# Performance work log

Hardware: AMD Instinct MI355X
Metric: run time of the kernel (lower is better)

The kernel has to match this reference:

```python
import jax, jax.numpy as jnp
import numpy as np

N_NODES = 50000
N_EDGES = 1250000
VOCAB = 50000
EMBED = 64
HIDDEN = 64
NUM_REL = 3
N_CLASSES = 2
N_GRAPHS = 512


def setup_inputs() -> dict:
    key = jax.random.key(0)
    ks = jax.random.split(key, 12)
    x = jax.random.randint(ks[0], (N_NODES,), 0, VOCAB, dtype=jnp.int32)
    edge_index = jax.random.randint(ks[1], (2, N_EDGES), 0, N_NODES, dtype=jnp.int32)
    edge_type = jax.random.randint(ks[2], (N_EDGES,), 0, NUM_REL, dtype=jnp.int32)
    batch = jnp.sort(jax.random.randint(ks[3], (N_NODES,), 0, N_GRAPHS, dtype=jnp.int32))
    s = 0.05
    emb = jax.random.normal(ks[4], (VOCAB, EMBED), jnp.float32) * s
    w1_rel = jax.random.normal(ks[5], (NUM_REL, EMBED, HIDDEN), jnp.float32) * s
    w1_root = jax.random.normal(ks[6], (EMBED, HIDDEN), jnp.float32) * s
    b1 = jnp.zeros((HIDDEN,), jnp.float32)
    w2_rel = jax.random.normal(ks[7], (NUM_REL, HIDDEN, HIDDEN), jnp.float32) * s
    w2_root = jax.random.normal(ks[8], (HIDDEN, HIDDEN), jnp.float32) * s
    b2 = jnp.zeros((HIDDEN,), jnp.float32)
    lin_w = jax.random.normal(ks[9], (HIDDEN, N_CLASSES), jnp.float32) * s
    lin_b = jnp.zeros((N_CLASSES,), jnp.float32)
    return {"x": x, "edge_index": edge_index, "edge_type": edge_type, "batch": batch,
            "emb": emb, "w1_rel": w1_rel, "w1_root": w1_root, "b1": b1,
            "w2_rel": w2_rel, "w2_root": w2_root, "b2": b2,
            "lin_w": lin_w, "lin_b": lin_b}


def rgcn_conv(h, src, dst, edge_type, w_rel, w_root, bias):
    # PyG RGCNConv: out = h @ W_root + bias + sum_r mean-aggregated (h_src @ W_r)
    out = h @ w_root + bias
    h_src = h[src]  # [E, F] gather
    for r in range(NUM_REL):
        mask = (edge_type == r).astype(h.dtype)  # [E]
        m = (h_src @ w_rel[r]) * mask[:, None]   # [E, H]
        s = jax.ops.segment_sum(m, dst, num_segments=N_NODES)
        cnt = jax.ops.segment_sum(mask, dst, num_segments=N_NODES)
        out = out + s / jnp.maximum(cnt, 1.0)[:, None]
    return out


def reference(x, edge_index, edge_type, batch, emb, w1_rel, w1_root, b1,
              w2_rel, w2_root, b2, lin_w, lin_b):
    src, dst = edge_index[0], edge_index[1]
    emb_eff = emb.at[0].set(0.0)  # padding_idx=0
    h = emb_eff[x]  # [N, EMBED]
    h = jax.nn.relu(rgcn_conv(h, src, dst, edge_type, w1_rel, w1_root, b1))
    h = jax.nn.relu(rgcn_conv(h, src, dst, edge_type, w2_rel, w2_root, b2))
    # global mean pool over graphs
    sums = jax.ops.segment_sum(h, batch, num_segments=N_GRAPHS)
    cnt = jax.ops.segment_sum(jnp.ones((h.shape[0],), h.dtype), batch, num_segments=N_GRAPHS)
    pooled = sums / jnp.maximum(cnt, 1.0)[:, None]  # [G, HIDDEN]
    return pooled @ lin_w + lin_b  # [G, N_CLASSES]
```

## Files before the change

kernel.cpp:

```cpp
#include <hip/hip_runtime.h>

#define CHUNK 2048

__global__ __launch_bounds__(256) void embed_count_kernel(
    const int* __restrict__ x, const float* __restrict__ emb, float* __restrict__ h0,
    const int* __restrict__ ei, int* __restrict__ pcount,
    int n_nodes, int n_edges, int n_bkt, int embed_blocks)
{
    __shared__ int cnt[512];
    int t = threadIdx.x;
    if ((int)blockIdx.x < embed_blocks) {
        int tt = blockIdx.x * 256 + t;
        if (tt < n_nodes * 16) {
            int n = tt >> 4, q = tt & 15;
            int xv = x[n];
            float4 v = {0.f, 0.f, 0.f, 0.f};
            if (xv != 0) v = *(const float4*)(emb + (size_t)xv * 64 + q * 4);
            *(float4*)(h0 + (size_t)n * 64 + q * 4) = v;
        }
        return;
    }
    int jb = blockIdx.x - embed_blocks;
    for (int b = t; b < 512; b += 256) cnt[b] = 0;
    __syncthreads();
    int base = jb * CHUNK;
#pragma unroll
    for (int i = 0; i < CHUNK / 256; ++i) {
        int e = base + i * 256 + t;
        if (e < n_edges) atomicAdd(&cnt[ei[n_edges + e] >> 7], 1);
    }
    __syncthreads();
    for (int b = t; b < n_bkt; b += 256) pcount[jb * n_bkt + b] = cnt[b];
}

__global__ __launch_bounds__(256) void colscan_kernel(
    const int* __restrict__ pcount, int* __restrict__ pre,
    int* __restrict__ totals, int* __restrict__ rowstartR,
    const int* __restrict__ batch, const float* __restrict__ linb,
    float* __restrict__ inv_cnt, float* __restrict__ outg,
    int n_chk, int n_bkt, int n_edges, int n_nodes, int n_graphs)
{
    __shared__ int ps[256];
    int b = blockIdx.x, t = threadIdx.x;
    if (b >= n_bkt) {
        int g = (b - n_bkt) * 256 + t;
        if (g < n_graphs) {
            int lo = 0, hi = n_nodes;
            while (lo < hi) { int mid = (lo + hi) >> 1; if (batch[mid] < g) lo = mid + 1; else hi = mid; }
            int s = lo;
            lo = 0; hi = n_nodes;
            while (lo < hi) { int mid = (lo + hi) >> 1; if (batch[mid] < g + 1) lo = mid + 1; else hi = mid; }
            inv_cnt[g] = 1.f / (float)max(lo - s, 1);
            outg[2 * g + 0] = linb[0];
            outg[2 * g + 1] = linb[1];
        }
        return;
    }
    if (b == 0 && t == 0) rowstartR[4 * n_nodes] = n_edges;
    int v[4], s = 0;
#pragma unroll
    for (int i = 0; i < 4; ++i) {
        int jj = t * 4 + i;
        v[i] = (jj < n_chk) ? pcount[jj * n_bkt + b] : 0;
        s += v[i];
    }
    ps[t] = s;
    __syncthreads();
    for (int o = 1; o < 256; o <<= 1) {
        int u = (t >= o) ? ps[t - o] : 0;
        __syncthreads();
        ps[t] += u;
        __syncthreads();
    }
    int run = (t > 0) ? ps[t - 1] : 0;
#pragma unroll
    for (int i = 0; i < 4; ++i) {
        int jj = t * 4 + i;
        if (jj < n_chk) pre[jj * n_bkt + b] = run;
        run += v[i];
    }
    if (t == 255) totals[b] = run;
}

__global__ __launch_bounds__(256) void scatter_kernel(
    const int* __restrict__ ei, const int* __restrict__ et,
    const int* __restrict__ pre, const int* __restrict__ totals,
    int* __restrict__ esort, int* __restrict__ bucket_start,
    int n_edges, int n_bkt)
{
    __shared__ int bs[512], fill2[512], ps[256];
    int t = threadIdx.x, j = blockIdx.x;
    int a0 = (2 * t < n_bkt) ? totals[2 * t] : 0;
    int a1 = (2 * t + 1 < n_bkt) ? totals[2 * t + 1] : 0;
    ps[t] = a0 + a1;
    __syncthreads();
    for (int o = 1; o < 256; o <<= 1) {
        int u = (t >= o) ? ps[t - o] : 0;
        __syncthreads();
        ps[t] += u;
        __syncthreads();
    }
    int basex = (t > 0) ? ps[t - 1] : 0;
    bs[2 * t] = basex;
    bs[2 * t + 1] = basex + a0;
    fill2[t] = 0; fill2[t + 256] = 0;
    __syncthreads();
    if (j == 0) {
        for (int b = t; b < n_bkt; b += 256) bucket_start[b] = bs[b];
        if (t == 0) bucket_start[n_bkt] = n_edges;
    }
    for (int b = t; b < n_bkt; b += 256) bs[b] += pre[j * n_bkt + b];
    __syncthreads();
    int base = j * CHUNK;
#pragma unroll
    for (int i = 0; i < CHUNK / 256; ++i) {
        int e = base + i * 256 + t;
        if (e < n_edges) {
            int s = ei[e], d = ei[n_edges + e], r = et[e];
            int b = d >> 7;
            int pos = bs[b] + atomicAdd(&fill2[b], 1);
            esort[pos] = s | (r << 16) | ((d & 127) << 18);
        }
    }
}

__global__ __launch_bounds__(256) void bucket_sort_kernel(
    const int* __restrict__ bucket_start, int* __restrict__ esort,
    int* __restrict__ scratch, int* __restrict__ rowstartR, int n_nodes)
{
    __shared__ int cnt[512], off[512], fill[512], ps[256];
    int t = threadIdx.x, b = blockIdx.x;
    int s = bucket_start[b], e = bucket_start[b + 1];
    cnt[t] = 0; cnt[t + 256] = 0; fill[t] = 0; fill[t + 256] = 0;
    __syncthreads();
    int* scr = scratch + (size_t)b * 8192;
    for (int i = s + t; i < e; i += 256) {
        int p = esort[i];
        scr[i - s] = p;
        atomicAdd(&cnt[(p >> 16) & 0x1FF], 1);
    }
    __syncthreads();
    int a0 = cnt[2 * t], a1 = cnt[2 * t + 1];
    ps[t] = a0 + a1;
    __syncthreads();
    for (int o = 1; o < 256; o <<= 1) {
        int v = (t >= o) ? ps[t - o] : 0;
        __syncthreads();
        ps[t] += v;
        __syncthreads();
    }
    int basex = (t > 0) ? ps[t - 1] : 0;
    off[2 * t] = basex;
    off[2 * t + 1] = basex + a0;
    __syncthreads();
    int d0 = b * 128 + (2 * t >> 2);
    if (d0 < n_nodes) rowstartR[b * 512 + 2 * t] = s + off[2 * t];
    int d1 = b * 128 + ((2 * t + 1) >> 2);
    if (d1 < n_nodes) rowstartR[b * 512 + 2 * t + 1] = s + off[2 * t + 1];
    __syncthreads();
    for (int i = s + t; i < e; i += 256) {
        int p = scr[i - s];
        int bin = (p >> 16) & 0x1FF;
        int pos = s + off[bin] + atomicAdd(&fill[bin], 1);
        esort[pos] = p;
    }
}

__global__ __launch_bounds__(256) void agg_kernel(
    const float* __restrict__ hin, const int* __restrict__ rowstartR,
    const int* __restrict__ esort, float* __restrict__ means, int n_nodes)
{
    int wid = (blockIdx.x * 256 + threadIdx.x) >> 6;
    int lane = threadIdx.x & 63;
    if (wid >= n_nodes) return;
    int q = lane >> 4;
    int c = lane & 15;
    int4 rs = *(const int4*)(rowstartR + wid * 4);
    int s = rs.x, e = rs.w;

    float4 a0 = {0.f,0.f,0.f,0.f}, a1 = {0.f,0.f,0.f,0.f}, a2 = {0.f,0.f,0.f,0.f};

    int i = s + 4 * q;
    for (; i + 4 <= e; i += 16) {
        int p0 = esort[i], p1 = esort[i + 1], p2 = esort[i + 2], p3 = esort[i + 3];
        float4 v0 = *(const float4*)(hin + (size_t)(p0 & 0xFFFF) * 64 + c * 4);
        float4 v1 = *(const float4*)(hin + (size_t)(p1 & 0xFFFF) * 64 + c * 4);
        float4 v2 = *(const float4*)(hin + (size_t)(p2 & 0xFFFF) * 64 + c * 4);
        float4 v3 = *(const float4*)(hin + (size_t)(p3 & 0xFFFF) * 64 + c * 4);
#pragma unroll
        for (int m = 0; m < 4; ++m) {
            int p = m == 0 ? p0 : m == 1 ? p1 : m == 2 ? p2 : p3;
            float4 v = m == 0 ? v0 : m == 1 ? v1 : m == 2 ? v2 : v3;
            int r = (p >> 16) & 3;
            float m0 = (r == 0) ? 1.f : 0.f;
            float m1 = (r == 1) ? 1.f : 0.f;
            float m2 = (r == 2) ? 1.f : 0.f;
            a0.x = fmaf(m0, v.x, a0.x); a0.y = fmaf(m0, v.y, a0.y);
            a0.z = fmaf(m0, v.z, a0.z); a0.w = fmaf(m0, v.w, a0.w);
            a1.x = fmaf(m1, v.x, a1.x); a1.y = fmaf(m1, v.y, a1.y);
            a1.z = fmaf(m1, v.z, a1.z); a1.w = fmaf(m1, v.w, a1.w);
            a2.x = fmaf(m2, v.x, a2.x); a2.y = fmaf(m2, v.y, a2.y);
            a2.z = fmaf(m2, v.z, a2.z); a2.w = fmaf(m2, v.w, a2.w);
        }
    }
#pragma unroll
    for (int m = 0; m < 3; ++m) {
        int ii = i + m;
        if (ii < e) {
            int p = esort[ii];
            float4 v = *(const float4*)(hin + (size_t)(p & 0xFFFF) * 64 + c * 4);
            int r = (p >> 16) & 3;
            float m0 = (r == 0) ? 1.f : 0.f;
            float m1 = (r == 1) ? 1.f : 0.f;
            float m2 = (r == 2) ? 1.f : 0.f;
            a0.x = fmaf(m0, v.x, a0.x); a0.y = fmaf(m0, v.y, a0.y);
            a0.z = fmaf(m0, v.z, a0.z); a0.w = fmaf(m0, v.w, a0.w);
            a1.x = fmaf(m1, v.x, a1.x); a1.y = fmaf(m1, v.y, a1.y);
            a1.z = fmaf(m1, v.z, a1.z); a1.w = fmaf(m1, v.w, a1.w);
            a2.x = fmaf(m2, v.x, a2.x); a2.y = fmaf(m2, v.y, a2.y);
            a2.z = fmaf(m2, v.z, a2.z); a2.w = fmaf(m2, v.w, a2.w);
        }
    }
#pragma unroll
    for (int off = 16; off < 64; off <<= 1) {
        a0.x += __shfl_xor(a0.x, off); a0.y += __shfl_xor(a0.y, off);
        a0.z += __shfl_xor(a0.z, off); a0.w += __shfl_xor(a0.w, off);
        a1.x += __shfl_xor(a1.x, off); a1.y += __shfl_xor(a1.y, off);
        a1.z += __shfl_xor(a1.z, off); a1.w += __shfl_xor(a1.w, off);
        a2.x += __shfl_xor(a2.x, off); a2.y += __shfl_xor(a2.y, off);
        a2.z += __shfl_xor(a2.z, off); a2.w += __shfl_xor(a2.w, off);
    }
    if (q < 3) {
        int cnt = (q == 0) ? (rs.y - rs.x) : (q == 1) ? (rs.z - rs.y) : (rs.w - rs.z);
        float4 a = (q == 0) ? a0 : (q == 1) ? a1 : a2;
        float inv = 1.f / (float)max(cnt, 1);
        float4 m = {a.x * inv, a.y * inv, a.z * inv, a.w * inv};
        *(float4*)(means + (size_t)wid * 192 + q * 64 + c * 4) = m;
    }
}

__global__ __launch_bounds__(256) void transform_kernel(
    const float* __restrict__ hin, const float* __restrict__ means,
    const float* __restrict__ wroot, const float* __restrict__ wrel,
    const float* __restrict__ bias, float* __restrict__ hout,
    const int* __restrict__ batch, const float* __restrict__ linw,
    const float* __restrict__ inv_cnt, float* __restrict__ outg,
    int n_nodes, int do_pool)
{
    __shared__ float wsh[2][4096];
    __shared__ float gacc[64][2];
    int t = threadIdx.x;
    int gt = blockIdx.x * 256 + t;
    int g = gt >> 4, q = gt & 15;
    int n0 = g * 4;
    bool active = (n0 < n_nodes);

    {
        const float4* sp = (const float4*)wroot;
        float4* d = (float4*)wsh[0];
#pragma unroll
        for (int i = 0; i < 4; ++i) d[t + i * 256] = sp[t + i * 256];
    }

    float4 acc[4];
    float4 b = {0.f, 0.f, 0.f, 0.f};
    if (active) b = *(const float4*)(bias + q * 4);
#pragma unroll
    for (int i = 0; i < 4; ++i) acc[i] = b;

    const float* hv = hin + (size_t)n0 * 64;
    const float* mv = means + (size_t)n0 * 192;

    for (int s = 0; s < 4; ++s) {
        __syncthreads();
        if (s < 3) {
            const float4* sp = (const float4*)wrel + (size_t)s * 1024;
            float4* d = (float4*)wsh[(s + 1) & 1];
#pragma unroll
            for (int i = 0; i < 4; ++i) d[t + i * 256] = sp[t + i * 256];
        }
        const float* vbase = (s == 0) ? hv : (mv + (s - 1) * 64);
        int vstride = (s == 0) ? 64 : 192;
        const float* wbuf = wsh[s & 1];
        if (active) {
#pragma unroll 4
            for (int k4 = 0; k4 < 16; ++k4) {
                float4 v[4];
#pragma unroll
                for (int i = 0; i < 4; ++i)
                    v[i] = *(const float4*)(vbase + i * vstride + k4 * 4);
#pragma unroll
                for (int kk = 0; kk < 4; ++kk) {
                    float4 w = *(const float4*)(wbuf + (k4 * 4 + kk) * 64 + q * 4);
#pragma unroll
                    for (int i = 0; i < 4; ++i) {
                        float sv = kk == 0 ? v[i].x : kk == 1 ? v[i].y : kk == 2 ? v[i].z : v[i].w;
                        acc[i].x = fmaf(sv, w.x, acc[i].x);
                        acc[i].y = fmaf(sv, w.y, acc[i].y);
                        acc[i].z = fmaf(sv, w.z, acc[i].z);
                        acc[i].w = fmaf(sv, w.w, acc[i].w);
                    }
                }
            }
        }
    }
    if (!do_pool) {
        if (active) {
            float* o = hout + (size_t)n0 * 64 + q * 4;
#pragma unroll
            for (int i = 0; i < 4; ++i) {
                float4 r = {fmaxf(acc[i].x, 0.f), fmaxf(acc[i].y, 0.f),
                            fmaxf(acc[i].z, 0.f), fmaxf(acc[i].w, 0.f)};
                *(float4*)(o + i * 64) = r;
            }
        }
    } else {
        if (t < 64) { gacc[t][0] = 0.f; gacc[t][1] = 0.f; }
        __syncthreads();
        int nbase = blockIdx.x * 64;
        int gmin = batch[min(nbase, n_nodes - 1)];
        if (active) {
            float4 lwA = *(const float4*)(linw + q * 8);
            float4 lwB = *(const float4*)(linw + q * 8 + 4);
            float d0[4], d1[4];
#pragma unroll
            for (int i = 0; i < 4; ++i) {
                float4 r = {fmaxf(acc[i].x, 0.f), fmaxf(acc[i].y, 0.f),
                            fmaxf(acc[i].z, 0.f), fmaxf(acc[i].w, 0.f)};
                d0[i] = r.x * lwA.x + r.y * lwA.z + r.z * lwB.x + r.w * lwB.z;
                d1[i] = r.x * lwA.y + r.y * lwA.w + r.z * lwB.y + r.w * lwB.w;
            }
#pragma unroll
            for (int off = 1; off < 16; off <<= 1) {
#pragma unroll
                for (int i = 0; i < 4; ++i) {
                    d0[i] += __shfl_xor(d0[i], off);
                    d1[i] += __shfl_xor(d1[i], off);
                }
            }
            if (q == 0) {
#pragma unroll
                for (int i = 0; i < 4; ++i) {
                    int n = n0 + i;
                    if (n < n_nodes) {
                        int gg = batch[n];
                        float ic = inv_cnt[gg];
                        int idx = gg - gmin;
                        if (idx < 64) {
                            atomicAdd(&gacc[idx][0], d0[i] * ic);
                            atomicAdd(&gacc[idx][1], d1[i] * ic);
                        } else {
                            atomicAdd(&outg[2 * gg + 0], d0[i] * ic);
                            atomicAdd(&outg[2 * gg + 1], d1[i] * ic);
                        }
                    }
                }
            }
        }
        __syncthreads();
        if (t < 64) {
            float v0 = gacc[t][0], v1 = gacc[t][1];
            if (v0 != 0.f || v1 != 0.f) {
                atomicAdd(&outg[2 * (gmin + t) + 0], v0);
                atomicAdd(&outg[2 * (gmin + t) + 1], v1);
            }
        }
    }
}

extern "C" void kernel_launch(void* const* d_in, const int* in_sizes, int n_in,
                              void* d_out, int out_size, void* d_ws, size_t ws_size,
                              hipStream_t stream)
{
    const int*   x      = (const int*)d_in[0];
    const int*   ei     = (const int*)d_in[1];
    const int*   et     = (const int*)d_in[2];
    const int*   batch  = (const int*)d_in[3];
    const float* emb    = (const float*)d_in[4];
    const float* w1rel  = (const float*)d_in[5];
    const float* w1root = (const float*)d_in[6];
    const float* b1     = (const float*)d_in[7];
    const float* w2rel  = (const float*)d_in[8];
    const float* w2root = (const float*)d_in[9];
    const float* b2     = (const float*)d_in[10];
    const float* linw   = (const float*)d_in[11];
    const float* linb   = (const float*)d_in[12];
    float* out = (float*)d_out;

    const int N = in_sizes[0];
    const int E = in_sizes[2];
    const int G = out_size / 2;
    const int NBKT = (N + 127) >> 7;
    const int NCHK = (E + CHUNK - 1) / CHUNK;

    float* hA        = (float*)d_ws;
    float* hB        = hA + (size_t)N * 64;
    float* means     = hB + (size_t)N * 64;
    int*   esort     = (int*)(means + (size_t)N * 192);
    int*   rowstartR = esort + E;
    int*   bucket_start = rowstartR + 4 * N + 4;
    int*   totals    = bucket_start + NBKT + 1;
    float* inv_cnt   = (float*)(totals + NBKT);
    int*   scratch   = (int*)means;
    int*   pcount    = (int*)means + 4 * 1024 * 1024;
    int*   pre       = (int*)means + 5 * 1024 * 1024;

    int embedBlocks = (N * 16 + 255) / 256;
    embed_count_kernel<<<embedBlocks + NCHK, 256, 0, stream>>>(
        x, emb, hA, ei, pcount, N, E, NBKT, embedBlocks);
    int gBlocks = (G + 255) / 256;
    colscan_kernel<<<NBKT + gBlocks, 256, 0, stream>>>(
        pcount, pre, totals, rowstartR, batch, linb, inv_cnt, out,
        NCHK, NBKT, E, N, G);
    scatter_kernel<<<NCHK, 256, 0, stream>>>(ei, et, pre, totals, esort, bucket_start, E, NBKT);
    bucket_sort_kernel<<<NBKT, 256, 0, stream>>>(bucket_start, esort, scratch, rowstartR, N);

    int aggBlocks = (N * 64 + 255) / 256;
    int tfBlocks  = ((N + 3) / 4 * 16 + 255) / 256;
    agg_kernel<<<aggBlocks, 256, 0, stream>>>(hA, rowstartR, esort, means, N);
    transform_kernel<<<tfBlocks, 256, 0, stream>>>(
        hA, means, w1root, w1rel, b1, hB, batch, linw, inv_cnt, out, N, 0);
    agg_kernel<<<aggBlocks, 256, 0, stream>>>(hB, rowstartR, esort, means, N);
    transform_kernel<<<tfBlocks, 256, 0, stream>>>(
        hB, means, w2root, w2rel, b2, hA, batch, linw, inv_cnt, out, N, 1);
}
```

Measured before the change: 308.5 us.

## Halve per-thread node tile in transform kernel and stage weights via direct LDS loads

The transform kernel now processes two nodes per 16-thread group instead of four, doubling the block count. Weights are staged in 32-row half-matrices through global_load_lds, which cuts shared memory per block from 32 KB to 16 KB, and the pipeline runs over 8 sub-stages. A launch-bounds occupancy hint of 6 is added. The goal is more occupancy and latency hiding, at the cost of less register reuse of weight loads and twice as many barriers.

```diff
diff --git a/kernel.cpp b/kernel.cpp
--- a/kernel.cpp
+++ b/kernel.cpp
@@ -239,7 +239,15 @@
     }
 }
 
-__global__ __launch_bounds__(256) void transform_kernel(
+__device__ __forceinline__ void stage16(const float* gsrc, float* ldst)
+{
+    __builtin_amdgcn_global_load_lds(
+        (const __attribute__((address_space(1))) unsigned int*)gsrc,
+        (__attribute__((address_space(3))) unsigned int*)ldst,
+        16, 0, 0);
+}
+
+__global__ __launch_bounds__(256, 6) void transform_kernel(
     const float* __restrict__ hin, const float* __restrict__ means,
     const float* __restrict__ wroot, const float* __restrict__ wrel,
     const float* __restrict__ bias, float* __restrict__ hout,
@@ -247,59 +255,58 @@
     const float* __restrict__ inv_cnt, float* __restrict__ outg,
     int n_nodes, int do_pool)
 {
-    __shared__ float wsh[2][4096];
+    __shared__ float wsh[2][2048];
     __shared__ float gacc[64][2];
     int t = threadIdx.x;
     int gt = blockIdx.x * 256 + t;
     int g = gt >> 4, q = gt & 15;
-    int n0 = g * 4;
+    int n0 = g * 2;
     bool active = (n0 < n_nodes);
 
+    stage16(wroot + t * 4,        wsh[0] + t * 4);
+    stage16(wroot + 1024 + t * 4, wsh[0] + 1024 + t * 4);
+
+    float4 acc0, acc1;
     {
-        const float4* sp = (const float4*)wroot;
-        float4* d = (float4*)wsh[0];
-#pragma unroll
-        for (int i = 0; i < 4; ++i) d[t + i * 256] = sp[t + i * 256];
-    }
-
-    float4 acc[4];
-    float4 b = {0.f, 0.f, 0.f, 0.f};
-    if (active) b = *(const float4*)(bias + q * 4);
-#pragma unroll
-    for (int i = 0; i < 4; ++i) acc[i] = b;
+        float4 b = {0.f, 0.f, 0.f, 0.f};
+        if (active) b = *(const float4*)(bias + q * 4);
+        acc0 = b; acc1 = b;
+    }
 
     const float* hv = hin + (size_t)n0 * 64;
     const float* mv = means + (size_t)n0 * 192;
 
-    for (int s = 0; s < 4; ++s) {
-        __syncthreads();
-        if (s < 3) {
-            const float4* sp = (const float4*)wrel + (size_t)s * 1024;
-            float4* d = (float4*)wsh[(s + 1) & 1];
-#pragma unroll
-            for (int i = 0; i < 4; ++i) d[t + i * 256] = sp[t + i * 256];
-        }
-        const float* vbase = (s == 0) ? hv : (mv + (s - 1) * 64);
-        int vstride = (s == 0) ? 64 : 192;
-        const float* wbuf = wsh[s & 1];
+    for (int ss = 0; ss < 8; ++ss) {
+        __syncthreads();
+        if (ss < 7) {
+            const float* wsrc = (ss + 1 < 2) ? (wroot + (size_t)(ss + 1) * 2048)
+                                             : (wrel + (size_t)(ss - 1) * 2048);
+            float* d = wsh[(ss + 1) & 1];
+            stage16(wsrc + t * 4,        d + t * 4);
+            stage16(wsrc + 1024 + t * 4, d + 1024 + t * 4);
+        }
+        int p = ss >> 1;
+        const float* vbase = ((p == 0) ? hv : (mv + (p - 1) * 64)) + (ss & 1) * 32;
+        int vstride = (p == 0) ? 64 : 192;
+        const float* wbuf = wsh[ss & 1];
         if (active) {
-#pragma unroll 4
-            for (int k4 = 0; k4 < 16; ++k4) {
-                float4 v[4];
-#pragma unroll
-                for (int i = 0; i < 4; ++i)
-                    v[i] = *(const float4*)(vbase + i * vstride + k4 * 4);
+#pragma unroll 2
+            for (int k4 = 0; k4 < 8; ++k4) {
+                float4 v0 = *(const float4*)(vbase + k4 * 4);
+                float4 v1 = *(const float4*)(vbase + vstride + k4 * 4);
 #pragma unroll
                 for (int kk = 0; kk < 4; ++kk) {
                     float4 w = *(const float4*)(wbuf + (k4 * 4 + kk) * 64 + q * 4);
-#pragma unroll
-                    for (int i = 0; i < 4; ++i) {
-                        float sv = kk == 0 ? v[i].x : kk == 1 ? v[i].y : kk == 2 ? v[i].z : v[i].w;
-                        acc[i].x = fmaf(sv, w.x, acc[i].x);
-                        acc[i].y = fmaf(sv, w.y, acc[i].y);
-                        acc[i].z = fmaf(sv, w.z, acc[i].z);
-                        acc[i].w = fmaf(sv, w.w, acc[i].w);
-                    }
+                    float s0 = kk == 0 ? v0.x : kk == 1 ? v0.y : kk == 2 ? v0.z : v0.w;
+                    float s1 = kk == 0 ? v1.x : kk == 1 ? v1.y : kk == 2 ? v1.z : v1.w;
+                    acc0.x = fmaf(s0, w.x, acc0.x);
+                    acc0.y = fmaf(s0, w.y, acc0.y);
+                    acc0.z = fmaf(s0, w.z, acc0.z);
+                    acc0.w = fmaf(s0, w.w, acc0.w);
+                    acc1.x = fmaf(s1, w.x, acc1.x);
+                    acc1.y = fmaf(s1, w.y, acc1.y);
+                    acc1.z = fmaf(s1, w.z, acc1.z);
+                    acc1.w = fmaf(s1, w.w, acc1.w);
                 }
             }
         }
@@ -307,40 +314,45 @@
     if (!do_pool) {
         if (active) {
             float* o = hout + (size_t)n0 * 64 + q * 4;
-#pragma unroll
-            for (int i = 0; i < 4; ++i) {
-                float4 r = {fmaxf(acc[i].x, 0.f), fmaxf(acc[i].y, 0.f),
-                            fmaxf(acc[i].z, 0.f), fmaxf(acc[i].w, 0.f)};
-                *(float4*)(o + i * 64) = r;
-            }
+            float4 r0 = {fmaxf(acc0.x, 0.f), fmaxf(acc0.y, 0.f),
+                         fmaxf(acc0.z, 0.f), fmaxf(acc0.w, 0.f)};
+            float4 r1 = {fmaxf(acc1.x, 0.f), fmaxf(acc1.y, 0.f),
+                         fmaxf(acc1.z, 0.f), fmaxf(acc1.w, 0.f)};
+            *(float4*)(o) = r0;
+            *(float4*)(o + 64) = r1;
         }
     } else {
         if (t < 64) { gacc[t][0] = 0.f; gacc[t][1] = 0.f; }
         __syncthreads();
-        int nbase = blockIdx.x * 64;
+        int nbase = blockIdx.x * 32;
         int gmin = batch[min(nbase, n_nodes - 1)];
         if (active) {
             float4 lwA = *(const float4*)(linw + q * 8);
             float4 lwB = *(const float4*)(linw + q * 8 + 4);
-            float d0[4], d1[4];
-#pragma unroll
-            for (int i = 0; i < 4; ++i) {
-                float4 r = {fmaxf(acc[i].x, 0.f), fmaxf(acc[i].y, 0.f),
-                            fmaxf(acc[i].z, 0.f), fmaxf(acc[i].w, 0.f)};
-                d0[i] = r.x * lwA.x + r.y * lwA.z + r.z * lwB.x + r.w * lwB.z;
-                d1[i] = r.x * lwA.y + r.y * lwA.w + r.z * lwB.y + r.w * lwB.w;
+            float d0[2], d1[2];
+            {
+                float4 r = {fmaxf(acc0.x, 0.f), fmaxf(acc0.y, 0.f),
+                            fmaxf(acc0.z, 0.f), fmaxf(acc0.w, 0.f)};
+                d0[0] = r.x * lwA.x + r.y * lwA.z + r.z * lwB.x + r.w * lwB.z;
+                d1[0] = r.x * lwA.y + r.y * lwA.w + r.z * lwB.y + r.w * lwB.w;
+            }
+            {
+                float4 r = {fmaxf(acc1.x, 0.f), fmaxf(acc1.y, 0.f),
+                            fmaxf(acc1.z, 0.f), fmaxf(acc1.w, 0.f)};
+                d0[1] = r.x * lwA.x + r.y * lwA.z + r.z * lwB.x + r.w * lwB.z;
+                d1[1] = r.x * lwA.y + r.y * lwA.w + r.z * lwB.y + r.w * lwB.w;
             }
 #pragma unroll
             for (int off = 1; off < 16; off <<= 1) {
 #pragma unroll
-                for (int i = 0; i < 4; ++i) {
+                for (int i = 0; i < 2; ++i) {
                     d0[i] += __shfl_xor(d0[i], off);
                     d1[i] += __shfl_xor(d1[i], off);
                 }
             }
             if (q == 0) {
 #pragma unroll
-                for (int i = 0; i < 4; ++i) {
+                for (int i = 0; i < 2; ++i) {
                     int n = n0 + i;
                     if (n < n_nodes) {
                         int gg = batch[n];
@@ -416,7 +428,7 @@
     bucket_sort_kernel<<<NBKT, 256, 0, stream>>>(bucket_start, esort, scratch, rowstartR, N);
 
     int aggBlocks = (N * 64 + 255) / 256;
-    int tfBlocks  = ((N + 3) / 4 * 16 + 255) / 256;
+    int tfBlocks  = ((N + 1) / 2 * 16 + 255) / 256;
     agg_kernel<<<aggBlocks, 256, 0, stream>>>(hA, rowstartR, esort, means, N);
     transform_kernel<<<tfBlocks, 256, 0, stream>>>(
         hA, means, w1root, w1rel, b1, hB, batch, linw, inv_cnt, out, N, 0);
```

New measurement: 299.4 us. 1.03x faster.
